# Kernel tuning notes

Hardware: AMD Instinct MI355X
Metric: run time of the kernel (lower is better)

## Reference

```python
import jax, jax.numpy as jnp
import numpy as np

N_NODES = 100000
N_EDGES = 1600000
D = 64
K = 10


def setup_inputs() -> dict:
    key = jax.random.key(0)
    k1, k2, k3, k4 = jax.random.split(key, 4)
    features = jax.random.normal(k1, (N_NODES, D), dtype=jnp.float32)
    s = jax.random.normal(k2, (D, 1), dtype=jnp.float32)
    src = jax.random.randint(k3, (N_EDGES,), 0, N_NODES, dtype=jnp.int64)
    dst = jax.random.randint(k4, (N_EDGES,), 0, N_NODES, dtype=jnp.int64)
    return {"features": features, "s": s, "src": src, "dst": dst, "k": K}


def reference(features, s, src, dst, k):
    n = features.shape[0]
    # symmetric degree norm: deg_in clamped at 1, norm = deg^{-1/2}
    deg = jax.ops.segment_sum(jnp.ones_like(dst, dtype=features.dtype), dst,
                              num_segments=n)
    norm = jnp.power(jnp.maximum(deg, 1.0), -0.5)[:, None]  # [N,1]

    def step(h, _):
        h = h * norm
        # copy_u + sum: scatter-add src features into dst nodes (SpMM)
        h = jax.ops.segment_sum(h[src], dst, num_segments=n)
        h = h * norm
        return h, h

    _, hops = jax.lax.scan(step, features, None, length=k)  # [k,N,D]
    H = jnp.concatenate([features[None], hops], axis=0)      # [k+1,N,D]
    H = jnp.transpose(H, (1, 0, 2))                           # [N,k+1,D]
    # attention pooling: S = sigmoid(H @ s), out = S^T H
    S = jax.nn.sigmoid(jnp.einsum('nkd,d->nk', H, s[:, 0]))  # [N,k+1]
    out = jnp.einsum('nk,nkd->nd', S, H)                      # [N,D]
    return out
```

## Files before the change

kernel.cpp:

```cpp
#include <hip/hip_runtime.h>
#include <hip/hip_fp16.h>
#include <math.h>

#define D 64
#define RB 1024
#define EB 2048
#define NRMAX 128
#define KHOPS 10


typedef union { uint4 u; __half2 h[4]; } U4H;


__global__ void countA(const int* __restrict__ dst, int* __restrict__ countsA_T,
                       int E, int NR, int NBLK) {
    __shared__ int hist[NRMAX];
    int t = threadIdx.x;
    for (int i = t; i < NR; i += 256) hist[i] = 0;
    __syncthreads();
    int base = blockIdx.x * EB + t;
    #pragma unroll
    for (int j = 0; j < EB / 256; ++j) {
        int e = base + j * 256;
        if (e < E) atomicAdd(&hist[dst[e] >> 10], 1);
    }
    __syncthreads();
    for (int i = t; i < NR; i += 256) countsA_T[i * NBLK + blockIdx.x] = hist[i];
}

__global__ void block_sums(const int* __restrict__ arr, int* __restrict__ bsum, int n) {
    int base = blockIdx.x * 1024;
    int t = threadIdx.x;
    int v = 0;
    #pragma unroll
    for (int j = 0; j < 4; ++j) {
        int i = base + t + j * 256;
        if (i < n) v += arr[i];
    }
    #pragma unroll
    for (int m = 32; m >= 1; m >>= 1) v += __shfl_xor(v, m, 64);
    __shared__ int ws[4];
    if ((t & 63) == 0) ws[t >> 6] = v;
    __syncthreads();
    if (t == 0) bsum[blockIdx.x] = ws[0] + ws[1] + ws[2] + ws[3];
}

__global__ void scan_bsums(int* __restrict__ bsum, int nb) {
    __shared__ int tmp[1024];
    int t = threadIdx.x;
    int v = (t < nb) ? bsum[t] : 0;
    tmp[t] = v;
    __syncthreads();
    for (int off = 1; off < 1024; off <<= 1) {
        int x = (t >= off) ? tmp[t - off] : 0;
        __syncthreads();
        tmp[t] += x;
        __syncthreads();
    }
    if (t < nb) bsum[t] = tmp[t] - v;
}

__global__ void gen_scan2(const int* __restrict__ arr, const int* __restrict__ bsum,
                          int* __restrict__ out, int n) {
    __shared__ int tmp[1024];
    int base = blockIdx.x * 1024;
    int t = threadIdx.x;
    int i = base + t;
    int v = (i < n) ? arr[i] : 0;
    tmp[t] = v;
    __syncthreads();
    for (int off = 1; off < 1024; off <<= 1) {
        int x = (t >= off) ? tmp[t - off] : 0;
        __syncthreads();
        tmp[t] += x;
        __syncthreads();
    }
    if (i < n) out[i] = bsum[blockIdx.x] + tmp[t] - v;
}

__global__ void passA2(const int* __restrict__ src, const int* __restrict__ dst,
                       const int* __restrict__ baseA, unsigned int* __restrict__ ebuf2,
                       int E, int NR, int NBLK) {
    __shared__ int cur[NRMAX];
    int t = threadIdx.x;
    for (int i = t; i < NR; i += 256) cur[i] = baseA[i * NBLK + blockIdx.x];
    __syncthreads();
    int base = blockIdx.x * EB + t;
    #pragma unroll
    for (int j = 0; j < EB / 256; ++j) {
        int e = base + j * 256;
        if (e < E) {
            int v = dst[e];
            int pos = atomicAdd(&cur[v >> 10], 1);
            ebuf2[pos] = (unsigned int)src[e] | ((unsigned int)(v & (RB - 1)) << 17);
        }
    }
}

__global__ void range_build(const unsigned int* __restrict__ ebuf2,
                            const int* __restrict__ baseA,
                            int* __restrict__ offsets, float* __restrict__ norm,
                            int* __restrict__ csr, int N, int E, int NR, int NBLK) {
    __shared__ int cnt[RB];
    __shared__ int sc[RB];
    int rg = blockIdx.x;
    int t = threadIdx.x;
    int r0 = baseA[rg * NBLK];
    int r1 = (rg + 1 < NR) ? baseA[(rg + 1) * NBLK] : E;
    cnt[t] = 0;
    __syncthreads();
    for (int i = r0 + t; i < r1; i += RB)
        atomicAdd(&cnt[ebuf2[i] >> 17], 1);
    __syncthreads();
    int v = cnt[t];
    sc[t] = v;
    __syncthreads();
    for (int off = 1; off < RB; off <<= 1) {
        int x = (t >= off) ? sc[t - off] : 0;
        __syncthreads();
        sc[t] += x;
        __syncthreads();
    }
    int excl = sc[t] - v;
    int node = rg * RB + t;
    if (node < N) {
        offsets[node] = r0 + excl;
        norm[node] = rsqrtf((float)(v > 1 ? v : 1));
    }
    if (rg == NR - 1 && t == 0) offsets[N] = E;
    __syncthreads();
    cnt[t] = r0 + excl;
    __syncthreads();
    for (int i = r0 + t; i < r1; i += RB) {
        unsigned int u = ebuf2[i];
        int pos = atomicAdd(&cnt[u >> 17], 1);
        csr[pos] = (int)(u & 0x1FFFFu);
    }
}


__global__ void hop0(const float4* __restrict__ feat, const float* __restrict__ s,
                     const float* __restrict__ norm, uint4* __restrict__ g0,
                     float4* __restrict__ out, int n, int do_pool) {
    int t = blockIdx.x * blockDim.x + threadIdx.x;
    int node = t >> 3;
    int l = t & 7;
    if (node > n) return;
    if (node == n) {
        g0[(size_t)n * 8 + l] = make_uint4(0u, 0u, 0u, 0u);
        return;
    }
    float4 f0 = feat[node * 16 + 2 * l];
    float4 f1 = feat[node * 16 + 2 * l + 1];
    float nv = norm[node];
    U4H P;
    P.h[0] = __floats2half2_rn(f0.x * nv, f0.y * nv);
    P.h[1] = __floats2half2_rn(f0.z * nv, f0.w * nv);
    P.h[2] = __floats2half2_rn(f1.x * nv, f1.y * nv);
    P.h[3] = __floats2half2_rn(f1.z * nv, f1.w * nv);
    g0[(size_t)node * 8 + l] = P.u;
    if (do_pool) {
        const float4* s4 = (const float4*)s;
        float4 a = s4[2 * l], b = s4[2 * l + 1];
        float dot = f0.x * a.x + f0.y * a.y + f0.z * a.z + f0.w * a.w
                  + f1.x * b.x + f1.y * b.y + f1.z * b.z + f1.w * b.w;
        #pragma unroll
        for (int m = 1; m <= 4; m <<= 1) dot += __shfl_xor(dot, m, 64);
        float sig = 1.0f / (1.0f + expf(-dot));
        out[node * 16 + 2 * l]     = make_float4(sig * f0.x, sig * f0.y, sig * f0.z, sig * f0.w);
        out[node * 16 + 2 * l + 1] = make_float4(sig * f1.x, sig * f1.y, sig * f1.z, sig * f1.w);
    }
}


__global__ __launch_bounds__(256, 8)
void spmm_hop(const uint4* __restrict__ gin, const int* __restrict__ offsets,
              const int* __restrict__ csr, const float* __restrict__ norm,
              const float* __restrict__ s, uint4* __restrict__ gout,
              float4* __restrict__ out, int n, int do_pool, int write_g) {
    int lane = threadIdx.x & 63;
    int node = __builtin_amdgcn_readfirstlane(blockIdx.x * 4 + (threadIdx.x >> 6));
    if (node > n) return;
    int g = lane >> 3;
    int l = lane & 7;
    if (node == n) {
        if (write_g && g == 0) gout[(size_t)n * 8 + l] = make_uint4(0u, 0u, 0u, 0u);
        return;
    }
    int beg = offsets[node], end = offsets[node + 1];
    int deg = end - beg;
    int dcap = deg < 32 ? deg : 32;
    int idx = (lane < dcap) ? csr[beg + lane] : n;

    int u0 = __shfl(idx, g,      64);
    int u1 = __shfl(idx, g + 8,  64);
    int u2 = __shfl(idx, g + 16, 64);
    int u3 = __shfl(idx, g + 24, 64);
    U4H A0, A1, A2, A3;
    A0.u = gin[(size_t)u0 * 8 + l];
    A1.u = gin[(size_t)u1 * 8 + l];
    A2.u = gin[(size_t)u2 * 8 + l];
    A3.u = gin[(size_t)u3 * 8 + l];
    __builtin_amdgcn_sched_barrier(0);

    __half2 ah0, ah1, ah2, ah3;
    ah0 = __hadd2(A0.h[0], A1.h[0]); ah1 = __hadd2(A0.h[1], A1.h[1]);
    ah2 = __hadd2(A0.h[2], A1.h[2]); ah3 = __hadd2(A0.h[3], A1.h[3]);
    ah0 = __hadd2(ah0, A2.h[0]);     ah1 = __hadd2(ah1, A2.h[1]);
    ah2 = __hadd2(ah2, A2.h[2]);     ah3 = __hadd2(ah3, A2.h[3]);
    ah0 = __hadd2(ah0, A3.h[0]);     ah1 = __hadd2(ah1, A3.h[1]);
    ah2 = __hadd2(ah2, A3.h[2]);     ah3 = __hadd2(ah3, A3.h[3]);

    float2 q0 = __half22float2(ah0), q1 = __half22float2(ah1);
    float2 q2 = __half22float2(ah2), q3 = __half22float2(ah3);
    float acc[8] = {q0.x, q0.y, q1.x, q1.y, q2.x, q2.y, q3.x, q3.y};

    for (int i = beg + 32 + g; i < end; i += 8) {
        U4H P; P.u = gin[(size_t)csr[i] * 8 + l];
        float2 a0 = __half22float2(P.h[0]), a1 = __half22float2(P.h[1]);
        float2 a2 = __half22float2(P.h[2]), a3 = __half22float2(P.h[3]);
        acc[0] += a0.x; acc[1] += a0.y; acc[2] += a1.x; acc[3] += a1.y;
        acc[4] += a2.x; acc[5] += a2.y; acc[6] += a3.x; acc[7] += a3.y;
    }

    #pragma unroll
    for (int m = 8; m <= 32; m <<= 1) {
        #pragma unroll
        for (int jj = 0; jj < 8; ++jj) acc[jj] += __shfl_xor(acc[jj], m, 64);
    }

    float nv = norm[node];
    float h[8];
    #pragma unroll
    for (int jj = 0; jj < 8; ++jj) h[jj] = acc[jj] * nv;

    float sig = 0.f;
    if (do_pool) {
        const float4* s4 = (const float4*)s;
        float4 a = s4[2 * l], b = s4[2 * l + 1];
        float dot = h[0] * a.x + h[1] * a.y + h[2] * a.z + h[3] * a.w
                  + h[4] * b.x + h[5] * b.y + h[6] * b.z + h[7] * b.w;
        #pragma unroll
        for (int m = 1; m <= 4; m <<= 1) dot += __shfl_xor(dot, m, 64);
        sig = 1.0f / (1.0f + expf(-dot));
    }

    if (g == 0) {
        if (write_g) {
            U4H P;
            P.h[0] = __floats2half2_rn(h[0] * nv, h[1] * nv);
            P.h[1] = __floats2half2_rn(h[2] * nv, h[3] * nv);
            P.h[2] = __floats2half2_rn(h[4] * nv, h[5] * nv);
            P.h[3] = __floats2half2_rn(h[6] * nv, h[7] * nv);
            gout[(size_t)node * 8 + l] = P.u;
        }
        if (do_pool) {
            float4 o0 = out[node * 16 + 2 * l];
            float4 o1 = out[node * 16 + 2 * l + 1];
            o0.x += sig * h[0]; o0.y += sig * h[1]; o0.z += sig * h[2]; o0.w += sig * h[3];
            o1.x += sig * h[4]; o1.y += sig * h[5]; o1.z += sig * h[6]; o1.w += sig * h[7];
            out[node * 16 + 2 * l]     = o0;
            out[node * 16 + 2 * l + 1] = o1;
        }
    }
}


__global__ void pool_epilogue(const uint4* __restrict__ gbase, size_t gstride,
                              const float* __restrict__ norm,
                              const float* __restrict__ s,
                              float4* __restrict__ out, int N) {
    int t0 = blockIdx.x * blockDim.x + threadIdx.x;
    int node = t0 >> 3;
    int l = t0 & 7;
    if (node >= N) return;
    float inv_nv = 1.0f / norm[node];
    const float4* s4 = (const float4*)s;
    float4 sa = s4[2 * l], sb = s4[2 * l + 1];
    float o[8] = {0.f, 0.f, 0.f, 0.f, 0.f, 0.f, 0.f, 0.f};
    for (int t = 0; t <= KHOPS; ++t) {
        U4H P; P.u = gbase[(size_t)t * gstride + (size_t)node * 8 + l];
        float2 a0 = __half22float2(P.h[0]), a1 = __half22float2(P.h[1]);
        float2 a2 = __half22float2(P.h[2]), a3 = __half22float2(P.h[3]);
        float gf[8] = {a0.x, a0.y, a1.x, a1.y, a2.x, a2.y, a3.x, a3.y};
        float dot = gf[0] * sa.x + gf[1] * sa.y + gf[2] * sa.z + gf[3] * sa.w
                  + gf[4] * sb.x + gf[5] * sb.y + gf[6] * sb.z + gf[7] * sb.w;
        #pragma unroll
        for (int m = 1; m <= 4; m <<= 1) dot += __shfl_xor(dot, m, 64);
        float sig = 1.0f / (1.0f + expf(-dot * inv_nv));
        float sc = sig * inv_nv;
        #pragma unroll
        for (int j = 0; j < 8; ++j) o[j] += sc * gf[j];
    }
    out[node * 16 + 2 * l]     = make_float4(o[0], o[1], o[2], o[3]);
    out[node * 16 + 2 * l + 1] = make_float4(o[4], o[5], o[6], o[7]);
}


extern "C" void kernel_launch(void* const* d_in, const int* in_sizes, int n_in,
                              void* d_out, int out_size, void* d_ws, size_t ws_size,
                              hipStream_t stream) {
    const float* feat = (const float*)d_in[0];
    const float* s    = (const float*)d_in[1];
    const int*   src  = (const int*)d_in[2];
    const int*   dst  = (const int*)d_in[3];

    int N = in_sizes[0] / D;
    int E = in_sizes[2];
    int NR   = (N + RB - 1) / RB;
    int NBLK = (E + EB - 1) / EB;
    int M    = NR * NBLK;
    int nchA = (M + 1023) / 1024;

    int*   offsets  = (int*)d_ws;
    int*   csr      = offsets + (N + 1);
    float* norm     = (float*)(csr + E);
    int*   countsA  = (int*)(norm + N);
    int*   baseA    = countsA + M;
    int*   bsumA    = baseA + M;
    uintptr_t p = (uintptr_t)(bsumA + nchA);
    p = (p + 255) & ~(uintptr_t)255;
    uint4* gbase = (uint4*)p;
    size_t gstride = (size_t)(N + 1) * 8;

    size_t fixed_bytes = (uintptr_t)gbase - (uintptr_t)d_ws;
    int deferred = (ws_size >= fixed_bytes + (size_t)(KHOPS + 1) * gstride * sizeof(uint4)) ? 1 : 0;

    unsigned int* ebuf2 = (unsigned int*)(gbase + gstride);

    countA<<<NBLK, 256, 0, stream>>>(dst, countsA, E, NR, NBLK);
    block_sums<<<nchA, 256, 0, stream>>>(countsA, bsumA, M);
    scan_bsums<<<1, 1024, 0, stream>>>(bsumA, nchA);
    gen_scan2<<<nchA, 1024, 0, stream>>>(countsA, bsumA, baseA, M);
    passA2<<<NBLK, 256, 0, stream>>>(src, dst, baseA, ebuf2, E, NR, NBLK);
    range_build<<<NR, RB, 0, stream>>>(ebuf2, baseA, offsets, norm, csr, N, E, NR, NBLK);

    float4* outp = (float4*)d_out;
    int nb_node8 = ((N + 1) * 8 + 255) / 256;
    int nb_spmm  = (N + 4) / 4;

    hop0<<<nb_node8, 256, 0, stream>>>((const float4*)feat, s, norm, gbase,
                                       outp, N, deferred ? 0 : 1);

    if (deferred) {
        for (int t = 0; t < KHOPS; ++t) {
            spmm_hop<<<nb_spmm, 256, 0, stream>>>(
                gbase + (size_t)t * gstride, offsets, csr, norm, s,
                gbase + (size_t)(t + 1) * gstride, outp, N, 0, 1);
        }
        pool_epilogue<<<nb_node8, 256, 0, stream>>>(gbase, gstride, norm, s, outp, N);
    } else {
        uint4* gin = gbase;
        uint4* gout = gbase + gstride;
        for (int t = 0; t < KHOPS; ++t) {
            spmm_hop<<<nb_spmm, 256, 0, stream>>>(
                gin, offsets, csr, norm, s, gout, outp, N, 1, (t < KHOPS - 1) ? 1 : 0);
            uint4* tmp = gin; gin = gout; gout = tmp;
        }
    }
}
```

Before: 507.0 us.

## Make spmm_hop persistent and software-pipeline neighbor gathers across nodes

The SpMM hop kernel becomes a persistent grid-stride kernel with a fixed number of blocks, so each wave handles many nodes. Each wave issues the gathers for the next node's first 32 neighbors and prefetches the CSR indices two nodes ahead, all before it reduces the current node. The two sets of gather registers are ping-ponged to hide gather latency. In exchange, register use goes up, which is why launch bounds drop to 4 waves per SIMD, and the fixed grid size may balance load poorly.

New measurement: 587.3 us. +15.8%, slower.

```diff
diff --git a/kernel.cpp b/kernel.cpp
--- a/kernel.cpp
+++ b/kernel.cpp
@@ -7,6 +7,7 @@
 #define EB 2048
 #define NRMAX 128
 #define KHOPS 10
+#define SPMM_BLOCKS 2048
 
 
 typedef union { uint4 u; __half2 h[4]; } U4H;
@@ -173,95 +174,133 @@
 }
 
 
-__global__ __launch_bounds__(256, 8)
+#define CONSUME(C0, C1, C2, C3)                                               \
+    {                                                                         \
+        __half2 ah0, ah1, ah2, ah3;                                           \
+        ah0 = __hadd2(C0.h[0], C1.h[0]); ah1 = __hadd2(C0.h[1], C1.h[1]);     \
+        ah2 = __hadd2(C0.h[2], C1.h[2]); ah3 = __hadd2(C0.h[3], C1.h[3]);     \
+        ah0 = __hadd2(ah0, C2.h[0]);     ah1 = __hadd2(ah1, C2.h[1]);         \
+        ah2 = __hadd2(ah2, C2.h[2]);     ah3 = __hadd2(ah3, C2.h[3]);         \
+        ah0 = __hadd2(ah0, C3.h[0]);     ah1 = __hadd2(ah1, C3.h[1]);         \
+        ah2 = __hadd2(ah2, C3.h[2]);     ah3 = __hadd2(ah3, C3.h[3]);         \
+        float2 q0 = __half22float2(ah0), q1 = __half22float2(ah1);            \
+        float2 q2 = __half22float2(ah2), q3 = __half22float2(ah3);            \
+        float acc[8] = {q0.x, q0.y, q1.x, q1.y, q2.x, q2.y, q3.x, q3.y};      \
+        for (int i = begC + 32 + g; i < endC; i += 8) {                       \
+            U4H P; P.u = gin[(size_t)csr[i] * 8 + l];                         \
+            float2 a0 = __half22float2(P.h[0]), a1 = __half22float2(P.h[1]);  \
+            float2 a2 = __half22float2(P.h[2]), a3 = __half22float2(P.h[3]);  \
+            acc[0] += a0.x; acc[1] += a0.y; acc[2] += a1.x; acc[3] += a1.y;   \
+            acc[4] += a2.x; acc[5] += a2.y; acc[6] += a3.x; acc[7] += a3.y;   \
+        }                                                                     \
+        _Pragma("unroll")                                                     \
+        for (int m = 8; m <= 32; m <<= 1) {                                   \
+            _Pragma("unroll")                                                 \
+            for (int jj = 0; jj < 8; ++jj) acc[jj] += __shfl_xor(acc[jj], m, 64); \
+        }                                                                     \
+        float nv = norm[cur];                                                 \
+        float h0 = acc[0] * nv, h1 = acc[1] * nv, h2 = acc[2] * nv, h3 = acc[3] * nv; \
+        float h4 = acc[4] * nv, h5 = acc[5] * nv, h6 = acc[6] * nv, h7 = acc[7] * nv; \
+        float sig = 0.f;                                                      \
+        if (do_pool) {                                                        \
+            float dot = h0 * sa.x + h1 * sa.y + h2 * sa.z + h3 * sa.w         \
+                      + h4 * sb.x + h5 * sb.y + h6 * sb.z + h7 * sb.w;        \
+            _Pragma("unroll")                                                 \
+            for (int m = 1; m <= 4; m <<= 1) dot += __shfl_xor(dot, m, 64);   \
+            sig = 1.0f / (1.0f + expf(-dot));                                 \
+        }                                                                     \
+        if (g == 0) {                                                         \
+            if (write_g) {                                                    \
+                U4H P;                                                        \
+                P.h[0] = __floats2half2_rn(h0 * nv, h1 * nv);                 \
+                P.h[1] = __floats2half2_rn(h2 * nv, h3 * nv);                 \
+                P.h[2] = __floats2half2_rn(h4 * nv, h5 * nv);                 \
+                P.h[3] = __floats2half2_rn(h6 * nv, h7 * nv);                 \
+                gout[(size_t)cur * 8 + l] = P.u;                              \
+            }                                                                 \
+            if (do_pool) {                                                    \
+                float4 o0 = out[cur * 16 + 2 * l];                            \
+                float4 o1 = out[cur * 16 + 2 * l + 1];                        \
+                o0.x += sig * h0; o0.y += sig * h1; o0.z += sig * h2; o0.w += sig * h3; \
+                o1.x += sig * h4; o1.y += sig * h5; o1.z += sig * h6; o1.w += sig * h7; \
+                out[cur * 16 + 2 * l]     = o0;                               \
+                out[cur * 16 + 2 * l + 1] = o1;                               \
+            }                                                                 \
+        }                                                                     \
+    }
+
+#define BODY(IA0, IA1, IA2, IA3, IB0, IB1, IB2, IB3)                          \
+    {                                                                         \
+        int u0 = __shfl(idxN, g,      64);                                    \
+        int u1 = __shfl(idxN, g + 8,  64);                                    \
+        int u2 = __shfl(idxN, g + 16, 64);                                    \
+        int u3 = __shfl(idxN, g + 24, 64);                                    \
+        IB0.u = gin[(size_t)u0 * 8 + l];                                      \
+        IB1.u = gin[(size_t)u1 * 8 + l];                                      \
+        IB2.u = gin[(size_t)u2 * 8 + l];                                      \
+        IB3.u = gin[(size_t)u3 * 8 + l];                                      \
+        int nxt2 = nxt + W;                                                   \
+        int vn2 = (nxt2 < n);                                                 \
+        int bN2 = 0, eN2 = 0;                                                 \
+        if (vn2) { bN2 = offsets[nxt2]; eN2 = offsets[nxt2 + 1]; }            \
+        int dc2 = eN2 - bN2; if (dc2 > 32) dc2 = 32;                          \
+        int idx2 = (vn2 && lane < dc2) ? csr[bN2 + lane] : n;                 \
+        __builtin_amdgcn_sched_barrier(0);                                    \
+        CONSUME(IA0, IA1, IA2, IA3)                                           \
+        if (!vn) break;                                                       \
+        cur = nxt; begC = bN; endC = eN;                                      \
+        nxt = nxt2; vn = vn2; bN = bN2; eN = eN2; idxN = idx2;                \
+    }
+
+__global__ __launch_bounds__(256, 4)
 void spmm_hop(const uint4* __restrict__ gin, const int* __restrict__ offsets,
               const int* __restrict__ csr, const float* __restrict__ norm,
               const float* __restrict__ s, uint4* __restrict__ gout,
               float4* __restrict__ out, int n, int do_pool, int write_g) {
     int lane = threadIdx.x & 63;
-    int node = __builtin_amdgcn_readfirstlane(blockIdx.x * 4 + (threadIdx.x >> 6));
-    if (node > n) return;
     int g = lane >> 3;
     int l = lane & 7;
-    if (node == n) {
-        if (write_g && g == 0) gout[(size_t)n * 8 + l] = make_uint4(0u, 0u, 0u, 0u);
-        return;
-    }
-    int beg = offsets[node], end = offsets[node + 1];
-    int deg = end - beg;
-    int dcap = deg < 32 ? deg : 32;
-    int idx = (lane < dcap) ? csr[beg + lane] : n;
-
-    int u0 = __shfl(idx, g,      64);
-    int u1 = __shfl(idx, g + 8,  64);
-    int u2 = __shfl(idx, g + 16, 64);
-    int u3 = __shfl(idx, g + 24, 64);
-    U4H A0, A1, A2, A3;
-    A0.u = gin[(size_t)u0 * 8 + l];
-    A1.u = gin[(size_t)u1 * 8 + l];
-    A2.u = gin[(size_t)u2 * 8 + l];
-    A3.u = gin[(size_t)u3 * 8 + l];
-    __builtin_amdgcn_sched_barrier(0);
-
-    __half2 ah0, ah1, ah2, ah3;
-    ah0 = __hadd2(A0.h[0], A1.h[0]); ah1 = __hadd2(A0.h[1], A1.h[1]);
-    ah2 = __hadd2(A0.h[2], A1.h[2]); ah3 = __hadd2(A0.h[3], A1.h[3]);
-    ah0 = __hadd2(ah0, A2.h[0]);     ah1 = __hadd2(ah1, A2.h[1]);
-    ah2 = __hadd2(ah2, A2.h[2]);     ah3 = __hadd2(ah3, A2.h[3]);
-    ah0 = __hadd2(ah0, A3.h[0]);     ah1 = __hadd2(ah1, A3.h[1]);
-    ah2 = __hadd2(ah2, A3.h[2]);     ah3 = __hadd2(ah3, A3.h[3]);
-
-    float2 q0 = __half22float2(ah0), q1 = __half22float2(ah1);
-    float2 q2 = __half22float2(ah2), q3 = __half22float2(ah3);
-    float acc[8] = {q0.x, q0.y, q1.x, q1.y, q2.x, q2.y, q3.x, q3.y};
-
-    for (int i = beg + 32 + g; i < end; i += 8) {
-        U4H P; P.u = gin[(size_t)csr[i] * 8 + l];
-        float2 a0 = __half22float2(P.h[0]), a1 = __half22float2(P.h[1]);
-        float2 a2 = __half22float2(P.h[2]), a3 = __half22float2(P.h[3]);
-        acc[0] += a0.x; acc[1] += a0.y; acc[2] += a1.x; acc[3] += a1.y;
-        acc[4] += a2.x; acc[5] += a2.y; acc[6] += a3.x; acc[7] += a3.y;
-    }
-
-    #pragma unroll
-    for (int m = 8; m <= 32; m <<= 1) {
-        #pragma unroll
-        for (int jj = 0; jj < 8; ++jj) acc[jj] += __shfl_xor(acc[jj], m, 64);
-    }
-
-    float nv = norm[node];
-    float h[8];
-    #pragma unroll
-    for (int jj = 0; jj < 8; ++jj) h[jj] = acc[jj] * nv;
-
-    float sig = 0.f;
+    int wid = __builtin_amdgcn_readfirstlane((int)blockIdx.x * 4 + (threadIdx.x >> 6));
+    int W = (int)gridDim.x * 4;
+
+    if (write_g && wid == 0 && g == 0)
+        gout[(size_t)n * 8 + l] = make_uint4(0u, 0u, 0u, 0u);
+
+    float4 sa = make_float4(0.f, 0.f, 0.f, 0.f), sb = sa;
     if (do_pool) {
         const float4* s4 = (const float4*)s;
-        float4 a = s4[2 * l], b = s4[2 * l + 1];
-        float dot = h[0] * a.x + h[1] * a.y + h[2] * a.z + h[3] * a.w
-                  + h[4] * b.x + h[5] * b.y + h[6] * b.z + h[7] * b.w;
-        #pragma unroll
-        for (int m = 1; m <= 4; m <<= 1) dot += __shfl_xor(dot, m, 64);
-        sig = 1.0f / (1.0f + expf(-dot));
-    }
-
-    if (g == 0) {
-        if (write_g) {
-            U4H P;
-            P.h[0] = __floats2half2_rn(h[0] * nv, h[1] * nv);
-            P.h[1] = __floats2half2_rn(h[2] * nv, h[3] * nv);
-            P.h[2] = __floats2half2_rn(h[4] * nv, h[5] * nv);
-            P.h[3] = __floats2half2_rn(h[6] * nv, h[7] * nv);
-            gout[(size_t)node * 8 + l] = P.u;
-        }
-        if (do_pool) {
-            float4 o0 = out[node * 16 + 2 * l];
-            float4 o1 = out[node * 16 + 2 * l + 1];
-            o0.x += sig * h[0]; o0.y += sig * h[1]; o0.z += sig * h[2]; o0.w += sig * h[3];
-            o1.x += sig * h[4]; o1.y += sig * h[5]; o1.z += sig * h[6]; o1.w += sig * h[7];
-            out[node * 16 + 2 * l]     = o0;
-            out[node * 16 + 2 * l + 1] = o1;
-        }
+        sa = s4[2 * l]; sb = s4[2 * l + 1];
+    }
+
+    int cur = wid;
+    if (cur >= n) return;
+
+    int begC = offsets[cur], endC = offsets[cur + 1];
+    int dcC = endC - begC; if (dcC > 32) dcC = 32;
+    int idxC = (lane < dcC) ? csr[begC + lane] : n;
+
+    int nxt = cur + W;
+    int vn = (nxt < n);
+    int bN = 0, eN = 0;
+    if (vn) { bN = offsets[nxt]; eN = offsets[nxt + 1]; }
+    int dcN = eN - bN; if (dcN > 32) dcN = 32;
+
+    U4H A0, A1, A2, A3, B0, B1, B2, B3;
+    {
+        int u0 = __shfl(idxC, g,      64);
+        int u1 = __shfl(idxC, g + 8,  64);
+        int u2 = __shfl(idxC, g + 16, 64);
+        int u3 = __shfl(idxC, g + 24, 64);
+        A0.u = gin[(size_t)u0 * 8 + l];
+        A1.u = gin[(size_t)u1 * 8 + l];
+        A2.u = gin[(size_t)u2 * 8 + l];
+        A3.u = gin[(size_t)u3 * 8 + l];
+    }
+    int idxN = (vn && lane < dcN) ? csr[bN + lane] : n;
+
+    for (;;) {
+        BODY(A0, A1, A2, A3, B0, B1, B2, B3)
+        BODY(B0, B1, B2, B3, A0, A1, A2, A3)
     }
 }
 
@@ -337,7 +376,7 @@
 
     float4* outp = (float4*)d_out;
     int nb_node8 = ((N + 1) * 8 + 255) / 256;
-    int nb_spmm  = (N + 4) / 4;
+    int nb_spmm  = SPMM_BLOCKS;
 
     hop0<<<nb_node8, 256, 0, stream>>>((const float4*)feat, s, norm, gbase,
                                        outp, N, deferred ? 0 : 1);
```

## Make SpMM hop kernel persistent with software-prefetched CSR offsets and indices

Applied to the files above, without the earlier changes.

Replaces the one-wave-per-node launch with a fixed grid of 2048 blocks where each wave loops over nodes with a grid stride. While gathering the current node's neighbour features, it prefetches the next node's neighbour indices and the offsets of the node after that, to hide index-load latency. It also hoists the attention vector load out of the loop. The trade-off is fewer resident waves relative to nodes and extra live registers, which could reduce latency hiding through occupancy.

Measured after the change: 536.3 us. +5.8%, slower.

```diff
diff --git a/kernel.cpp b/kernel.cpp
--- a/kernel.cpp
+++ b/kernel.cpp
@@ -7,6 +7,7 @@
 #define EB 2048
 #define NRMAX 128
 #define KHOPS 10
+#define SPMM_BLOCKS 2048
 
 
 typedef union { uint4 u; __half2 h[4]; } U4H;
@@ -179,89 +180,111 @@
               const float* __restrict__ s, uint4* __restrict__ gout,
               float4* __restrict__ out, int n, int do_pool, int write_g) {
     int lane = threadIdx.x & 63;
-    int node = __builtin_amdgcn_readfirstlane(blockIdx.x * 4 + (threadIdx.x >> 6));
-    if (node > n) return;
     int g = lane >> 3;
     int l = lane & 7;
-    if (node == n) {
-        if (write_g && g == 0) gout[(size_t)n * 8 + l] = make_uint4(0u, 0u, 0u, 0u);
-        return;
-    }
-    int beg = offsets[node], end = offsets[node + 1];
-    int deg = end - beg;
-    int dcap = deg < 32 ? deg : 32;
-    int idx = (lane < dcap) ? csr[beg + lane] : n;
-
-    int u0 = __shfl(idx, g,      64);
-    int u1 = __shfl(idx, g + 8,  64);
-    int u2 = __shfl(idx, g + 16, 64);
-    int u3 = __shfl(idx, g + 24, 64);
-    U4H A0, A1, A2, A3;
-    A0.u = gin[(size_t)u0 * 8 + l];
-    A1.u = gin[(size_t)u1 * 8 + l];
-    A2.u = gin[(size_t)u2 * 8 + l];
-    A3.u = gin[(size_t)u3 * 8 + l];
-    __builtin_amdgcn_sched_barrier(0);
-
-    __half2 ah0, ah1, ah2, ah3;
-    ah0 = __hadd2(A0.h[0], A1.h[0]); ah1 = __hadd2(A0.h[1], A1.h[1]);
-    ah2 = __hadd2(A0.h[2], A1.h[2]); ah3 = __hadd2(A0.h[3], A1.h[3]);
-    ah0 = __hadd2(ah0, A2.h[0]);     ah1 = __hadd2(ah1, A2.h[1]);
-    ah2 = __hadd2(ah2, A2.h[2]);     ah3 = __hadd2(ah3, A2.h[3]);
-    ah0 = __hadd2(ah0, A3.h[0]);     ah1 = __hadd2(ah1, A3.h[1]);
-    ah2 = __hadd2(ah2, A3.h[2]);     ah3 = __hadd2(ah3, A3.h[3]);
-
-    float2 q0 = __half22float2(ah0), q1 = __half22float2(ah1);
-    float2 q2 = __half22float2(ah2), q3 = __half22float2(ah3);
-    float acc[8] = {q0.x, q0.y, q1.x, q1.y, q2.x, q2.y, q3.x, q3.y};
-
-    for (int i = beg + 32 + g; i < end; i += 8) {
-        U4H P; P.u = gin[(size_t)csr[i] * 8 + l];
-        float2 a0 = __half22float2(P.h[0]), a1 = __half22float2(P.h[1]);
-        float2 a2 = __half22float2(P.h[2]), a3 = __half22float2(P.h[3]);
-        acc[0] += a0.x; acc[1] += a0.y; acc[2] += a1.x; acc[3] += a1.y;
-        acc[4] += a2.x; acc[5] += a2.y; acc[6] += a3.x; acc[7] += a3.y;
-    }
-
-    #pragma unroll
-    for (int m = 8; m <= 32; m <<= 1) {
-        #pragma unroll
-        for (int jj = 0; jj < 8; ++jj) acc[jj] += __shfl_xor(acc[jj], m, 64);
-    }
-
-    float nv = norm[node];
-    float h[8];
-    #pragma unroll
-    for (int jj = 0; jj < 8; ++jj) h[jj] = acc[jj] * nv;
-
-    float sig = 0.f;
+    int wid = __builtin_amdgcn_readfirstlane((int)blockIdx.x * 4 + (threadIdx.x >> 6));
+    int W = (int)gridDim.x * 4;
+
+    if (write_g && wid == 0 && g == 0)
+        gout[(size_t)n * 8 + l] = make_uint4(0u, 0u, 0u, 0u);
+
+    float4 sa = make_float4(0.f, 0.f, 0.f, 0.f), sb = sa;
     if (do_pool) {
         const float4* s4 = (const float4*)s;
-        float4 a = s4[2 * l], b = s4[2 * l + 1];
-        float dot = h[0] * a.x + h[1] * a.y + h[2] * a.z + h[3] * a.w
-                  + h[4] * b.x + h[5] * b.y + h[6] * b.z + h[7] * b.w;
+        sa = s4[2 * l]; sb = s4[2 * l + 1];
+    }
+
+    int cur = wid;
+    if (cur >= n) return;
+
+    int beg = offsets[cur], end = offsets[cur + 1];
+    int dc = end - beg; if (dc > 32) dc = 32;
+    int idx = (lane < dc) ? csr[beg + lane] : n;
+
+    int nxt = cur + W;
+    int vn = (nxt < n);
+    int b1 = 0, e1 = 0;
+    if (vn) { b1 = offsets[nxt]; e1 = offsets[nxt + 1]; }
+
+    for (;;) {
+        int u0 = __shfl(idx, g,      64);
+        int u1 = __shfl(idx, g + 8,  64);
+        int u2 = __shfl(idx, g + 16, 64);
+        int u3 = __shfl(idx, g + 24, 64);
+        U4H A0, A1, A2, A3;
+        A0.u = gin[(size_t)u0 * 8 + l];
+        A1.u = gin[(size_t)u1 * 8 + l];
+        A2.u = gin[(size_t)u2 * 8 + l];
+        A3.u = gin[(size_t)u3 * 8 + l];
+        int dc1 = e1 - b1; if (dc1 > 32) dc1 = 32;
+        int idx2 = (vn && lane < dc1) ? csr[b1 + lane] : n;
+        int nxt2 = nxt + W;
+        int vn2 = (nxt2 < n);
+        int b2 = 0, e2 = 0;
+        if (vn2) { b2 = offsets[nxt2]; e2 = offsets[nxt2 + 1]; }
+        __builtin_amdgcn_sched_barrier(0);
+
+        __half2 ah0, ah1, ah2, ah3;
+        ah0 = __hadd2(A0.h[0], A1.h[0]); ah1 = __hadd2(A0.h[1], A1.h[1]);
+        ah2 = __hadd2(A0.h[2], A1.h[2]); ah3 = __hadd2(A0.h[3], A1.h[3]);
+        ah0 = __hadd2(ah0, A2.h[0]);     ah1 = __hadd2(ah1, A2.h[1]);
+        ah2 = __hadd2(ah2, A2.h[2]);     ah3 = __hadd2(ah3, A2.h[3]);
+        ah0 = __hadd2(ah0, A3.h[0]);     ah1 = __hadd2(ah1, A3.h[1]);
+        ah2 = __hadd2(ah2, A3.h[2]);     ah3 = __hadd2(ah3, A3.h[3]);
+
+        float2 q0 = __half22float2(ah0), q1 = __half22float2(ah1);
+        float2 q2 = __half22float2(ah2), q3 = __half22float2(ah3);
+        float acc[8] = {q0.x, q0.y, q1.x, q1.y, q2.x, q2.y, q3.x, q3.y};
+
+        for (int i = beg + 32 + g; i < end; i += 8) {
+            U4H P; P.u = gin[(size_t)csr[i] * 8 + l];
+            float2 a0 = __half22float2(P.h[0]), a1 = __half22float2(P.h[1]);
+            float2 a2 = __half22float2(P.h[2]), a3 = __half22float2(P.h[3]);
+            acc[0] += a0.x; acc[1] += a0.y; acc[2] += a1.x; acc[3] += a1.y;
+            acc[4] += a2.x; acc[5] += a2.y; acc[6] += a3.x; acc[7] += a3.y;
+        }
+
         #pragma unroll
-        for (int m = 1; m <= 4; m <<= 1) dot += __shfl_xor(dot, m, 64);
-        sig = 1.0f / (1.0f + expf(-dot));
-    }
-
-    if (g == 0) {
-        if (write_g) {
-            U4H P;
-            P.h[0] = __floats2half2_rn(h[0] * nv, h[1] * nv);
-            P.h[1] = __floats2half2_rn(h[2] * nv, h[3] * nv);
-            P.h[2] = __floats2half2_rn(h[4] * nv, h[5] * nv);
-            P.h[3] = __floats2half2_rn(h[6] * nv, h[7] * nv);
-            gout[(size_t)node * 8 + l] = P.u;
-        }
+        for (int m = 8; m <= 32; m <<= 1) {
+            #pragma unroll
+            for (int jj = 0; jj < 8; ++jj) acc[jj] += __shfl_xor(acc[jj], m, 64);
+        }
+
+        float nv = norm[cur];
+        float h0 = acc[0] * nv, h1 = acc[1] * nv, h2 = acc[2] * nv, h3 = acc[3] * nv;
+        float h4 = acc[4] * nv, h5 = acc[5] * nv, h6 = acc[6] * nv, h7 = acc[7] * nv;
+
+        float sig = 0.f;
         if (do_pool) {
-            float4 o0 = out[node * 16 + 2 * l];
-            float4 o1 = out[node * 16 + 2 * l + 1];
-            o0.x += sig * h[0]; o0.y += sig * h[1]; o0.z += sig * h[2]; o0.w += sig * h[3];
-            o1.x += sig * h[4]; o1.y += sig * h[5]; o1.z += sig * h[6]; o1.w += sig * h[7];
-            out[node * 16 + 2 * l]     = o0;
-            out[node * 16 + 2 * l + 1] = o1;
-        }
+            float dot = h0 * sa.x + h1 * sa.y + h2 * sa.z + h3 * sa.w
+                      + h4 * sb.x + h5 * sb.y + h6 * sb.z + h7 * sb.w;
+            #pragma unroll
+            for (int m = 1; m <= 4; m <<= 1) dot += __shfl_xor(dot, m, 64);
+            sig = 1.0f / (1.0f + expf(-dot));
+        }
+
+        if (g == 0) {
+            if (write_g) {
+                U4H P;
+                P.h[0] = __floats2half2_rn(h0 * nv, h1 * nv);
+                P.h[1] = __floats2half2_rn(h2 * nv, h3 * nv);
+                P.h[2] = __floats2half2_rn(h4 * nv, h5 * nv);
+                P.h[3] = __floats2half2_rn(h6 * nv, h7 * nv);
+                gout[(size_t)cur * 8 + l] = P.u;
+            }
+            if (do_pool) {
+                float4 o0 = out[cur * 16 + 2 * l];
+                float4 o1 = out[cur * 16 + 2 * l + 1];
+                o0.x += sig * h0; o0.y += sig * h1; o0.z += sig * h2; o0.w += sig * h3;
+                o1.x += sig * h4; o1.y += sig * h5; o1.z += sig * h6; o1.w += sig * h7;
+                out[cur * 16 + 2 * l]     = o0;
+                out[cur * 16 + 2 * l + 1] = o1;
+            }
+        }
+
+        if (!vn) break;
+        cur = nxt; beg = b1; end = e1; idx = idx2;
+        nxt = nxt2; vn = vn2; b1 = b2; e1 = e2;
     }
 }
 
@@ -337,7 +360,7 @@
 
     float4* outp = (float4*)d_out;
     int nb_node8 = ((N + 1) * 8 + 255) / 256;
-    int nb_spmm  = (N + 4) / 4;
+    int nb_spmm  = SPMM_BLOCKS;
 
     hop0<<<nb_node8, 256, 0, stream>>>((const float4*)feat, s, norm, gbase,
                                        outp, N, deferred ? 0 : 1);
```

## Slice feature buffers by column quarter and pin slices to XCDs in SpMM

Applied to the files above, without the earlier changes.

Hop features are stored as four column slices of 16 halves each rather than one interleaved row. SpMM blocks are mapped so each XCD (block index mod 8) handles a single slice, which aims to keep each slice's gathered working set resident in that XCD's L2 and cut HBM traffic for the random neighbour gathers. It also adds a persistent grid-stride loop, half-precision partial reductions for low-degree nodes, and nontemporal loads and stores for the CSR indices and outputs. The costs are more index and lane-mapping logic, fp16 accumulation that loses some precision, and reliance on the hardware's round-robin dispatch of blocks to XCDs.

New measurement: 929.9 us. 83.4% more time.

```diff
diff --git a/kernel.cpp b/kernel.cpp
--- a/kernel.cpp
+++ b/kernel.cpp
@@ -7,9 +7,22 @@
 #define EB 2048
 #define NRMAX 128
 #define KHOPS 10
-
-
-typedef union { uint4 u; __half2 h[4]; } U4H;
+#define SLICES 4
+
+
+typedef unsigned int u32x4 __attribute__((ext_vector_type(4)));
+typedef union { u32x4 v; uint4 u; __half2 h[4]; int i[4]; } U4H;
+typedef union { __half2 h; int i; } H2I;
+
+__device__ __forceinline__ void nt_store16(uint4* p, u32x4 v) {
+    __builtin_nontemporal_store(v, (u32x4*)p);
+}
+__device__ __forceinline__ int nt_load_i32(const int* p) {
+    return __builtin_nontemporal_load(p);
+}
+__device__ __forceinline__ __half2 shfl_xor_h2(__half2 a, int m) {
+    H2I u; u.h = a; u.i = __shfl_xor(u.i, m, 64); return u.h;
+}
 
 
 __global__ void countA(const int* __restrict__ dst, int* __restrict__ countsA_T,
@@ -136,6 +149,156 @@
         int pos = atomicAdd(&cnt[u >> 17], 1);
         csr[pos] = (int)(u & 0x1FFFFu);
     }
+}
+
+
+__global__ void hop0_slice(const float4* __restrict__ feat,
+                           const float* __restrict__ norm,
+                           uint4* __restrict__ g0, int n) {
+    int t = blockIdx.x * blockDim.x + threadIdx.x;
+    int node = t >> 3;
+    int q = t & 7;
+    if (node > n) return;
+    size_t sl = (size_t)(n + 1) * 2;
+    uint4* dst = g0 + (size_t)(q >> 1) * sl + (size_t)node * 2 + (q & 1);
+    if (node == n) { *dst = make_uint4(0u, 0u, 0u, 0u); return; }
+    float4 f0 = feat[node * 16 + 2 * q];
+    float4 f1 = feat[node * 16 + 2 * q + 1];
+    float nv = norm[node];
+    U4H P;
+    P.h[0] = __floats2half2_rn(f0.x * nv, f0.y * nv);
+    P.h[1] = __floats2half2_rn(f0.z * nv, f0.w * nv);
+    P.h[2] = __floats2half2_rn(f1.x * nv, f1.y * nv);
+    P.h[3] = __floats2half2_rn(f1.z * nv, f1.w * nv);
+    *dst = P.u;
+}
+
+__global__ __launch_bounds__(256, 8)
+void spmm_slice(const uint4* __restrict__ gin, const int* __restrict__ offsets,
+                const int* __restrict__ csr, const float* __restrict__ norm,
+                uint4* __restrict__ gout, int n) {
+    int lane = threadIdx.x & 63;
+    int w = threadIdx.x >> 6;
+    int b = (int)blockIdx.x;
+    int xcd = b & 7;
+    int slice = xcd & 3;
+    int hi = xcd >> 2;
+    int j0 = b >> 3;
+    int sub = lane >> 5;
+    int r = lane & 31;
+    int e = r >> 1;
+    int hf = r & 1;
+
+    size_t sl = (size_t)(n + 1) * 2;
+    const uint4* gs = gin + (size_t)slice * sl;
+    uint4* os = gout + (size_t)slice * sl;
+
+    int G = (n + 8) >> 3;
+
+    for (int j = j0;; j += 256) {
+        int group = j * 2 + hi;
+        if (group >= G) break;
+        int node = group * 8 + w * 2 + sub;
+        bool live = (node < n);
+        int beg = 0, end = 0;
+        if (live) { beg = offsets[node]; end = offsets[node + 1]; }
+        int deg = end - beg;
+        int dcap = deg < 32 ? deg : 32;
+        int iA = (live && e < dcap)      ? nt_load_i32(&csr[beg + e])      : n;
+        int iB = (live && e + 16 < dcap) ? nt_load_i32(&csr[beg + e + 16]) : n;
+        U4H A, B;
+        A.u = gs[(size_t)iA * 2 + hf];
+        B.u = gs[(size_t)iB * 2 + hf];
+        __builtin_amdgcn_sched_barrier(0);
+
+        float f[8];
+        if (!__any(deg > 32)) {
+            __half2 a0 = __hadd2(A.h[0], B.h[0]);
+            __half2 a1 = __hadd2(A.h[1], B.h[1]);
+            __half2 a2 = __hadd2(A.h[2], B.h[2]);
+            __half2 a3 = __hadd2(A.h[3], B.h[3]);
+            a0 = __hadd2(a0, shfl_xor_h2(a0, 2));
+            a1 = __hadd2(a1, shfl_xor_h2(a1, 2));
+            a2 = __hadd2(a2, shfl_xor_h2(a2, 2));
+            a3 = __hadd2(a3, shfl_xor_h2(a3, 2));
+            float2 q0 = __half22float2(a0), q1 = __half22float2(a1);
+            float2 q2 = __half22float2(a2), q3 = __half22float2(a3);
+            f[0]=q0.x; f[1]=q0.y; f[2]=q1.x; f[3]=q1.y;
+            f[4]=q2.x; f[5]=q2.y; f[6]=q3.x; f[7]=q3.y;
+            #pragma unroll
+            for (int m = 4; m <= 16; m <<= 1) {
+                #pragma unroll
+                for (int jj = 0; jj < 8; ++jj) f[jj] += __shfl_xor(f[jj], m, 64);
+            }
+        } else {
+            float2 qa0 = __half22float2(A.h[0]), qa1 = __half22float2(A.h[1]);
+            float2 qa2 = __half22float2(A.h[2]), qa3 = __half22float2(A.h[3]);
+            float2 qb0 = __half22float2(B.h[0]), qb1 = __half22float2(B.h[1]);
+            float2 qb2 = __half22float2(B.h[2]), qb3 = __half22float2(B.h[3]);
+            f[0]=qa0.x+qb0.x; f[1]=qa0.y+qb0.y; f[2]=qa1.x+qb1.x; f[3]=qa1.y+qb1.y;
+            f[4]=qa2.x+qb2.x; f[5]=qa2.y+qb2.y; f[6]=qa3.x+qb3.x; f[7]=qa3.y+qb3.y;
+            for (int i = beg + 32 + e; i < end; i += 16) {
+                int ix = nt_load_i32(&csr[i]);
+                U4H P; P.u = gs[(size_t)ix * 2 + hf];
+                float2 p0 = __half22float2(P.h[0]), p1 = __half22float2(P.h[1]);
+                float2 p2 = __half22float2(P.h[2]), p3 = __half22float2(P.h[3]);
+                f[0]+=p0.x; f[1]+=p0.y; f[2]+=p1.x; f[3]+=p1.y;
+                f[4]+=p2.x; f[5]+=p2.y; f[6]+=p3.x; f[7]+=p3.y;
+            }
+            #pragma unroll
+            for (int m = 2; m <= 16; m <<= 1) {
+                #pragma unroll
+                for (int jj = 0; jj < 8; ++jj) f[jj] += __shfl_xor(f[jj], m, 64);
+            }
+        }
+
+        if ((lane & 30) == 0) {
+            if (node == n) {
+                os[(size_t)n * 2 + hf] = make_uint4(0u, 0u, 0u, 0u);
+            } else if (live) {
+                float nv = norm[node];
+                float s2 = nv * nv;
+                U4H P;
+                P.h[0] = __floats2half2_rn(f[0] * s2, f[1] * s2);
+                P.h[1] = __floats2half2_rn(f[2] * s2, f[3] * s2);
+                P.h[2] = __floats2half2_rn(f[4] * s2, f[5] * s2);
+                P.h[3] = __floats2half2_rn(f[6] * s2, f[7] * s2);
+                nt_store16(&os[(size_t)node * 2 + hf], P.v);
+            }
+        }
+    }
+}
+
+__global__ void pool_epilogue_slice(const uint4* __restrict__ gbase, size_t gstride,
+                                    const float* __restrict__ norm,
+                                    const float* __restrict__ s,
+                                    float4* __restrict__ out, int N) {
+    int t0 = blockIdx.x * blockDim.x + threadIdx.x;
+    int node = t0 >> 3;
+    int q = t0 & 7;
+    if (node >= N) return;
+    size_t sl = (size_t)(N + 1) * 2;
+    float inv_nv = 1.0f / norm[node];
+    const float4* s4 = (const float4*)s;
+    float4 sa = s4[2 * q], sb = s4[2 * q + 1];
+    float o[8] = {0.f, 0.f, 0.f, 0.f, 0.f, 0.f, 0.f, 0.f};
+    for (int t = 0; t <= KHOPS; ++t) {
+        U4H P; P.u = gbase[(size_t)t * gstride + (size_t)(q >> 1) * sl
+                           + (size_t)node * 2 + (q & 1)];
+        float2 a0 = __half22float2(P.h[0]), a1 = __half22float2(P.h[1]);
+        float2 a2 = __half22float2(P.h[2]), a3 = __half22float2(P.h[3]);
+        float gf[8] = {a0.x, a0.y, a1.x, a1.y, a2.x, a2.y, a3.x, a3.y};
+        float dot = gf[0] * sa.x + gf[1] * sa.y + gf[2] * sa.z + gf[3] * sa.w
+                  + gf[4] * sb.x + gf[5] * sb.y + gf[6] * sb.z + gf[7] * sb.w;
+        #pragma unroll
+        for (int m = 1; m <= 4; m <<= 1) dot += __shfl_xor(dot, m, 64);
+        float sig = 1.0f / (1.0f + expf(-dot * inv_nv));
+        float sc = sig * inv_nv;
+        #pragma unroll
+        for (int jj = 0; jj < 8; ++jj) o[jj] += sc * gf[jj];
+    }
+    out[node * 16 + 2 * q]     = make_float4(o[0], o[1], o[2], o[3]);
+    out[node * 16 + 2 * q + 1] = make_float4(o[4], o[5], o[6], o[7]);
 }
 
 
@@ -172,7 +335,6 @@
     }
 }
 
-
 __global__ __launch_bounds__(256, 8)
 void spmm_hop(const uint4* __restrict__ gin, const int* __restrict__ offsets,
               const int* __restrict__ csr, const float* __restrict__ norm,
@@ -266,37 +428,6 @@
 }
 
 
-__global__ void pool_epilogue(const uint4* __restrict__ gbase, size_t gstride,
-                              const float* __restrict__ norm,
-                              const float* __restrict__ s,
-                              float4* __restrict__ out, int N) {
-    int t0 = blockIdx.x * blockDim.x + threadIdx.x;
-    int node = t0 >> 3;
-    int l = t0 & 7;
-    if (node >= N) return;
-    float inv_nv = 1.0f / norm[node];
-    const float4* s4 = (const float4*)s;
-    float4 sa = s4[2 * l], sb = s4[2 * l + 1];
-    float o[8] = {0.f, 0.f, 0.f, 0.f, 0.f, 0.f, 0.f, 0.f};
-    for (int t = 0; t <= KHOPS; ++t) {
-        U4H P; P.u = gbase[(size_t)t * gstride + (size_t)node * 8 + l];
-        float2 a0 = __half22float2(P.h[0]), a1 = __half22float2(P.h[1]);
-        float2 a2 = __half22float2(P.h[2]), a3 = __half22float2(P.h[3]);
-        float gf[8] = {a0.x, a0.y, a1.x, a1.y, a2.x, a2.y, a3.x, a3.y};
-        float dot = gf[0] * sa.x + gf[1] * sa.y + gf[2] * sa.z + gf[3] * sa.w
-                  + gf[4] * sb.x + gf[5] * sb.y + gf[6] * sb.z + gf[7] * sb.w;
-        #pragma unroll
-        for (int m = 1; m <= 4; m <<= 1) dot += __shfl_xor(dot, m, 64);
-        float sig = 1.0f / (1.0f + expf(-dot * inv_nv));
-        float sc = sig * inv_nv;
-        #pragma unroll
-        for (int j = 0; j < 8; ++j) o[j] += sc * gf[j];
-    }
-    out[node * 16 + 2 * l]     = make_float4(o[0], o[1], o[2], o[3]);
-    out[node * 16 + 2 * l + 1] = make_float4(o[4], o[5], o[6], o[7]);
-}
-
-
 extern "C" void kernel_launch(void* const* d_in, const int* in_sizes, int n_in,
                               void* d_out, int out_size, void* d_ws, size_t ws_size,
                               hipStream_t stream) {
@@ -337,19 +468,19 @@
 
     float4* outp = (float4*)d_out;
     int nb_node8 = ((N + 1) * 8 + 255) / 256;
-    int nb_spmm  = (N + 4) / 4;
-
-    hop0<<<nb_node8, 256, 0, stream>>>((const float4*)feat, s, norm, gbase,
-                                       outp, N, deferred ? 0 : 1);
 
     if (deferred) {
+        hop0_slice<<<nb_node8, 256, 0, stream>>>((const float4*)feat, norm, gbase, N);
         for (int t = 0; t < KHOPS; ++t) {
-            spmm_hop<<<nb_spmm, 256, 0, stream>>>(
-                gbase + (size_t)t * gstride, offsets, csr, norm, s,
-                gbase + (size_t)(t + 1) * gstride, outp, N, 0, 1);
-        }
-        pool_epilogue<<<nb_node8, 256, 0, stream>>>(gbase, gstride, norm, s, outp, N);
+            spmm_slice<<<2048, 256, 0, stream>>>(
+                gbase + (size_t)t * gstride, offsets, csr, norm,
+                gbase + (size_t)(t + 1) * gstride, N);
+        }
+        pool_epilogue_slice<<<nb_node8, 256, 0, stream>>>(gbase, gstride, norm, s, outp, N);
     } else {
+        hop0<<<nb_node8, 256, 0, stream>>>((const float4*)feat, s, norm, gbase,
+                                           outp, N, 1);
+        int nb_spmm = (N + 4) / 4;
         uint4* gin = gbase;
         uint4* gout = gbase + gstride;
         for (int t = 0; t < KHOPS; ++t) {
```
